# Kernel optimization log

Measured on AMD Instinct MI355X. Metric: run time of the kernel, lower is better.

## Reference

```python
import jax, jax.numpy as jnp
import numpy as np

# Static conv config (matches init_kwargs)
STRIDE = (1, 1, 1)
PAD = (1, 1, 1)
DIL = (1, 1, 1)
DG = 1  # deformable groups


def setup_inputs() -> dict:
    key = jax.random.key(0)
    k1, k2, k3 = jax.random.split(key, 3)
    N, Cin, T, H, W = 2, 32, 8, 56, 56
    Cout, kT, kH, kW = 64, 3, 3, 3
    x = jax.random.normal(k1, (N, Cin, T, H, W), dtype=jnp.float32)
    # offset channels = DG * 3 * kT*kH*kW = 81 ; layout [N, dg*K*3, To, Ho, Wo]
    offset = jax.random.normal(k2, (N, DG * 3 * kT * kH * kW, T, H, W), dtype=jnp.float32)
    stdv = 1.0 / np.sqrt(Cin * kT * kH * kW)
    weight = jax.random.uniform(k3, (Cout, Cin, kT, kH, kW), dtype=jnp.float32, minval=-stdv, maxval=stdv)
    bias = jnp.zeros((Cout,), dtype=jnp.float32)
    return {"x": x, "offset": offset, "weight": weight, "bias": bias}


def _deform_conv3d(x, offset, weight, bias):
    N, C, T, H, W = x.shape
    Co, _, kT, kH, kW = weight.shape
    K = kT * kH * kW
    st, sh, sw = STRIDE
    pt_, ph_, pw_ = PAD
    dt_, dh_, dw_ = DIL
    To = (T + 2 * pt_ - (dt_ * (kT - 1) + 1)) // st + 1
    Ho = (H + 2 * ph_ - (dh_ * (kH - 1) + 1)) // sh + 1
    Wo = (W + 2 * pw_ - (dw_ * (kW - 1) + 1)) // sw + 1
    Cg = C // DG
    # offsets: [N, DG, K, 3(dt,dh,dw), To, Ho, Wo]
    off = offset.reshape(N, DG, K, 3, To, Ho, Wo)
    kt, kh, kw = [g.reshape(-1) for g in jnp.meshgrid(
        jnp.arange(kT), jnp.arange(kH), jnp.arange(kW), indexing='ij')]
    # base sampling grid per kernel tap: [K, To, Ho, Wo] via broadcasting
    bt = (jnp.arange(To) * st - pt_)[None, :, None, None] + (kt * dt_)[:, None, None, None]
    bh = (jnp.arange(Ho) * sh - ph_)[None, None, :, None] + (kh * dh_)[:, None, None, None]
    bw = (jnp.arange(Wo) * sw - pw_)[None, None, None, :] + (kw * dw_)[:, None, None, None]
    # fractional sampling positions: [N, DG, K, To, Ho, Wo]
    pt = bt[None, None] + off[:, :, :, 0]
    ph = bh[None, None] + off[:, :, :, 1]
    pw = bw[None, None] + off[:, :, :, 2]
    t0f, h0f, w0f = jnp.floor(pt), jnp.floor(ph), jnp.floor(pw)
    lt, lh, lw = pt - t0f, ph - h0f, pw - w0f
    t0 = t0f.astype(jnp.int32)
    h0 = h0f.astype(jnp.int32)
    w0 = w0f.astype(jnp.int32)
    x_flat = x.reshape(N, DG, Cg, T * H * W)
    acc = jnp.zeros((N, DG, Cg, K, To, Ho, Wo), dtype=x.dtype)
    for ct in (0, 1):
        ti = t0 + ct
        wt = lt if ct else (1.0 - lt)
        for ch in (0, 1):
            hi = h0 + ch
            wh = lh if ch else (1.0 - lh)
            for cw in (0, 1):
                wi = w0 + cw
                ww = lw if cw else (1.0 - lw)
                valid = ((ti >= 0) & (ti < T) & (hi >= 0) & (hi < H) & (wi >= 0) & (wi < W))
                idx = (jnp.clip(ti, 0, T - 1) * H + jnp.clip(hi, 0, H - 1)) * W + jnp.clip(wi, 0, W - 1)
                v = jnp.take_along_axis(x_flat, idx.reshape(N, DG, 1, -1), axis=3)
                v = v.reshape(N, DG, Cg, K, To, Ho, Wo)
                wgt = (wt * wh * ww * valid.astype(x.dtype))[:, :, None]  # [N,DG,1,K,To,Ho,Wo]
                acc = acc + v * wgt
    w_r = weight.reshape(Co, DG, Cg, K)
    out = jnp.einsum('ogck,ngcktuv->notuv', w_r, acc)
    if bias.size > 0:
        out = out + bias[None, :, None, None, None]
    return out


def reference(x, offset, weight, bias):
    return _deform_conv3d(x, offset, weight, bias)
```

## Files before the change

### kernel.cpp

```cpp
#include <hip/hip_runtime.h>
#include <hip/hip_fp16.h>

#define CIN   32
#define COUT  64
#define TT    8
#define HH    56
#define WW    56
#define KK    27
#define SP    (TT * HH * WW)
#define NB    2
#define NBLK  784
#define DBLK  1568
#define KSPLIT 14

typedef __attribute__((ext_vector_type(8))) _Float16 half8;
typedef __attribute__((ext_vector_type(4))) float    f32x4;

#define WF_OFF   0
#define XTH_OFF  (128 << 10)

__global__ __launch_bounds__(256) void prep_kernel(const float* __restrict__ x,
                                                   const float* __restrict__ w,
                                                   __half* __restrict__ xTh,
                                                   __half* __restrict__ wf) {
    const int b = blockIdx.x;
    const int t = threadIdx.x;
    if (b < NBLK) {
        __shared__ float sm[CIN][65];
        const int s0 = b * 64, n = s0 / SP, sp0 = s0 % SP;
#pragma unroll
        for (int it = 0; it < 8; ++it) {
            const int idx = it * 256 + t, c = idx >> 6, l = idx & 63;
            sm[c][l] = x[((size_t)n * CIN + c) * SP + sp0 + l];
        }
        __syncthreads();
#pragma unroll
        for (int it = 0; it < 4; ++it) {
            const int idx = it * 256 + t, l = idx >> 4, cp = idx & 15;
            ((__half2*)xTh)[((size_t)n * SP + sp0 + l) * (CIN / 2) + cp] =
                __floats2half2_rn(sm[2 * cp][l], sm[2 * cp + 1][l]);
        }
    } else {
        const int k = b - NBLK;
#pragma unroll
        for (int it = 0; it < 8; ++it) {
            const int idx  = it * 256 + t;
            const int j    = idx & 7;
            const int lane = (idx >> 3) & 63;
            const int ct   = (idx >> 9) & 3;
            const int co   = ct * 16 + (lane & 15);
            const int c    = (lane >> 4) * 8 + j;
            wf[(((size_t)k * 4 + ct) * 64 + lane) * 8 + j] =
                __float2half(w[((size_t)co * CIN + c) * KK + k]);
        }
    }
}

__global__ __launch_bounds__(256, 4) void dconv3d_kernel(const __half* __restrict__ xTh,
                                                         const float* __restrict__ off,
                                                         const __half* __restrict__ wf,
                                                         const float* __restrict__ bias,
                                                         float* __restrict__ out) {
    __shared__ __align__(16) char smem[81 * 32 * 4];
    float (*offs)[32] = reinterpret_cast<float(*)[32]>(smem);
    float (*cmb)[2][64] = reinterpret_cast<float(*)[2][64]>(smem);

    const int t    = threadIdx.x;
    const int lane = t & 63;
    const int wv   = t >> 6;
    const int wpos = wv & 1;
    const int half = wv >> 1;

    const int posI = lane >> 2;
    const int cgI  = lane & 3;
    const int jg   = lane >> 4;

    const int bp_addr = (((lane & 15) << 2) | jg) << 2;

    const int sb  = (blockIdx.x & 7) * 196 + (blockIdx.x >> 3);
    const int s0  = sb * 32;
    const int n   = s0 / SP;
    const int spb = s0 % SP;

    {
        const float* offbase = off + ((size_t)n * (3 * KK)) * SP + spb;
        for (int i = t; i < 81 * 8; i += 256) {
            const int row = i >> 3, q = i & 7;
            *(float4*)&offs[row][q * 4] = *(const float4*)(offbase + (size_t)row * SP + q * 4);
        }
    }
    __syncthreads();

    const int sp = spb + wpos * 16 + posI;
    const int to = sp / (HH * WW);
    const int hw = sp % (HH * WW);
    const int ho = hw / WW;
    const int wo = hw % WW;
    const int pl = wpos * 16 + posI;

    f32x4 acc[4];
#pragma unroll
    for (int ct = 0; ct < 4; ++ct)
#pragma unroll
        for (int r = 0; r < 4; ++r)
            acc[ct][r] = half ? 0.f : bias[ct * 16 + jg * 4 + r];

    const __half* xn = xTh + (size_t)n * SP * CIN;

    auto tap = [&](int k) {
        const int kt  = k / 9;
        const int khh = (k / 3) % 3;
        const int kww = k % 3;

        const float pt_ = (float)(to - 1 + kt)  + offs[k * 3 + 0][pl];
        const float ph_ = (float)(ho - 1 + khh) + offs[k * 3 + 1][pl];
        const float pw_ = (float)(wo - 1 + kww) + offs[k * 3 + 2][pl];

        const float ft = floorf(pt_), fh = floorf(ph_), fw = floorf(pw_);
        const float lt = pt_ - ft, lh = ph_ - fh, lw = pw_ - fw;
        const int t0 = (int)ft, h0 = (int)fh, w0 = (int)fw;
        const int t1 = t0 + 1, h1 = h0 + 1, w1 = w0 + 1;

        float awt[2], awh[2], aww[2];
        int   it2[2], ih2[2], iw2[2];
        awt[0] = ((unsigned)t0 < TT) ? (1.f - lt) : 0.f;
        awt[1] = ((unsigned)t1 < TT) ? lt : 0.f;
        it2[0] = min(max(t0, 0), TT - 1);  it2[1] = min(max(t1, 0), TT - 1);
        awh[0] = ((unsigned)h0 < HH) ? (1.f - lh) : 0.f;
        awh[1] = ((unsigned)h1 < HH) ? lh : 0.f;
        ih2[0] = min(max(h0, 0), HH - 1);  ih2[1] = min(max(h1, 0), HH - 1);
        aww[0] = ((unsigned)w0 < WW) ? (1.f - lw) : 0.f;
        aww[1] = ((unsigned)w1 < WW) ? lw : 0.f;
        iw2[0] = min(max(w0, 0), WW - 1);  iw2[1] = min(max(w1, 0), WW - 1);

        const int dT   = (it2[1] - it2[0]) * (HH * WW);
        const int dH   = (ih2[1] - ih2[0]) * WW;
        const int dW   = iw2[1] - iw2[0];
        const int base = (it2[0] * HH + ih2[0]) * WW + iw2[0];

        int   a[8];
        float cw[8];
        a[0] = base;           a[1] = base + dW;
        a[2] = base + dH;      a[3] = a[2] + dW;
        a[4] = base + dT;      a[5] = a[4] + dW;
        a[6] = a[4] + dH;      a[7] = a[6] + dW;
#pragma unroll
        for (int ci = 0; ci < 8; ++ci) {
            const int i0 = ci >> 2, i1 = (ci >> 1) & 1, i2 = ci & 1;
            cw[ci] = awt[i0] * awh[i1] * aww[i2];
        }

        float4 g[8];
#pragma unroll
        for (int ci = 0; ci < 8; ++ci)
            g[ci] = *(const float4*)(xn + (size_t)a[ci] * CIN + cgI * 8);

        __half2 vacc[4];
#pragma unroll
        for (int j = 0; j < 4; ++j) vacc[j] = __floats2half2_rn(0.f, 0.f);
#pragma unroll
        for (int ci = 0; ci < 8; ++ci) {
            const __half2* uh = (const __half2*)&g[ci];
            const __half2 cw2 = __float2half2_rn(cw[ci]);
            vacc[0] = __hfma2(cw2, uh[0], vacc[0]);
            vacc[1] = __hfma2(cw2, uh[1], vacc[1]);
            vacc[2] = __hfma2(cw2, uh[2], vacc[2]);
            vacc[3] = __hfma2(cw2, uh[3], vacc[3]);
        }

        union { __half2 h2[4]; int i[4]; half8 h8; } u, v;
#pragma unroll
        for (int d = 0; d < 4; ++d) u.h2[d] = vacc[d];
#pragma unroll
        for (int d = 0; d < 4; ++d)
            v.i[d] = __builtin_amdgcn_ds_bpermute(bp_addr, u.i[d]);
        const half8 bfrag = v.h8;

#pragma unroll
        for (int ct = 0; ct < 4; ++ct) {
            const half8 af = *(const half8*)(wf + (((size_t)k * 4 + ct) * 64 + lane) * 8);
            acc[ct] = __builtin_amdgcn_mfma_f32_16x16x32_f16(af, bfrag, acc[ct], 0, 0, 0);
        }
    };

    if (half == 0) {
#pragma unroll
        for (int k = 0; k < KSPLIT; ++k) tap(k);
    } else {
#pragma unroll
        for (int k = KSPLIT; k < KK; ++k) tap(k);
    }

    __syncthreads();
    if (half == 1) {
#pragma unroll
        for (int ct = 0; ct < 4; ++ct)
#pragma unroll
            for (int r = 0; r < 4; ++r) cmb[ct * 4 + r][wpos][lane] = acc[ct][r];
    }
    __syncthreads();
    if (half == 0) {
#pragma unroll
        for (int ct = 0; ct < 4; ++ct)
#pragma unroll
            for (int r = 0; r < 4; ++r) {
                const int co = ct * 16 + jg * 4 + r;
                out[((size_t)n * COUT + co) * SP + spb + wpos * 16 + (lane & 15)] =
                    acc[ct][r] + cmb[ct * 4 + r][wpos][lane];
            }
    }
}

extern "C" void kernel_launch(void* const* d_in, const int* in_sizes, int n_in,
                              void* d_out, int out_size, void* d_ws, size_t ws_size,
                              hipStream_t stream) {
    const float* x    = (const float*)d_in[0];
    const float* off  = (const float*)d_in[1];
    const float* w    = (const float*)d_in[2];
    const float* bias = (const float*)d_in[3];
    float* out        = (float*)d_out;

    __half* wf  = (__half*)((char*)d_ws + WF_OFF);
    __half* xTh = (__half*)((char*)d_ws + XTH_OFF);

    prep_kernel<<<NBLK + KK, 256, 0, stream>>>(x, w, xTh, wf);
    dconv3d_kernel<<<DBLK, 256, 0, stream>>>(xTh, off, wf, bias, out);
}
```

Measured before the change: 120.4 us.

## Split taps four ways per 16-position block and drop bpermute transpose

Each block now covers 16 output positions instead of 32, and its four waves each handle about a quarter of the 27 kernel taps. The grid doubles to 3136 blocks. Lanes now gather channels directly in the MFMA B-fragment layout (position = lane&15, channel group = lane>>4), which removes the ds_bpermute shuffle. The cost is a three-way LDS reduction at the end, more offset loads per output position, and uneven tap counts across waves (7,7,7,6).

```diff
diff --git a/kernel.cpp b/kernel.cpp
--- a/kernel.cpp
+++ b/kernel.cpp
@@ -10,8 +10,7 @@
 #define SP    (TT * HH * WW)
 #define NB    2
 #define NBLK  784
-#define DBLK  1568
-#define KSPLIT 14
+#define DBLK  3136
 
 typedef __attribute__((ext_vector_type(8))) _Float16 half8;
 typedef __attribute__((ext_vector_type(4))) float    f32x4;
@@ -61,49 +60,43 @@
                                                          const __half* __restrict__ wf,
                                                          const float* __restrict__ bias,
                                                          float* __restrict__ out) {
-    __shared__ __align__(16) char smem[81 * 32 * 4];
-    float (*offs)[32] = reinterpret_cast<float(*)[32]>(smem);
-    float (*cmb)[2][64] = reinterpret_cast<float(*)[2][64]>(smem);
+    __shared__ __align__(16) char smem[3 * 16 * 64 * 4];
+    float (*offs)[16]     = reinterpret_cast<float(*)[16]>(smem);
+    float (*cmb)[16][64]  = reinterpret_cast<float(*)[16][64]>(smem);
 
     const int t    = threadIdx.x;
     const int lane = t & 63;
-    const int wv   = t >> 6;
-    const int wpos = wv & 1;
-    const int half = wv >> 1;
-
-    const int posI = lane >> 2;
-    const int cgI  = lane & 3;
+    const int q    = t >> 6;
+
+    const int posI = lane & 15;
     const int jg   = lane >> 4;
 
-    const int bp_addr = (((lane & 15) << 2) | jg) << 2;
-
-    const int sb  = (blockIdx.x & 7) * 196 + (blockIdx.x >> 3);
-    const int s0  = sb * 32;
+    const int sb  = (blockIdx.x & 7) * 392 + (blockIdx.x >> 3);
+    const int s0  = sb * 16;
     const int n   = s0 / SP;
     const int spb = s0 % SP;
 
     {
         const float* offbase = off + ((size_t)n * (3 * KK)) * SP + spb;
-        for (int i = t; i < 81 * 8; i += 256) {
-            const int row = i >> 3, q = i & 7;
-            *(float4*)&offs[row][q * 4] = *(const float4*)(offbase + (size_t)row * SP + q * 4);
+        for (int i = t; i < 81 * 4; i += 256) {
+            const int row = i >> 2, qd = i & 3;
+            *(float4*)&offs[row][qd * 4] = *(const float4*)(offbase + (size_t)row * SP + qd * 4);
         }
     }
     __syncthreads();
 
-    const int sp = spb + wpos * 16 + posI;
+    const int sp = spb + posI;
     const int to = sp / (HH * WW);
     const int hw = sp % (HH * WW);
     const int ho = hw / WW;
     const int wo = hw % WW;
-    const int pl = wpos * 16 + posI;
 
     f32x4 acc[4];
 #pragma unroll
     for (int ct = 0; ct < 4; ++ct)
 #pragma unroll
         for (int r = 0; r < 4; ++r)
-            acc[ct][r] = half ? 0.f : bias[ct * 16 + jg * 4 + r];
+            acc[ct][r] = (q == 0) ? bias[ct * 16 + jg * 4 + r] : 0.f;
 
     const __half* xn = xTh + (size_t)n * SP * CIN;
 
@@ -112,9 +105,9 @@
         const int khh = (k / 3) % 3;
         const int kww = k % 3;
 
-        const float pt_ = (float)(to - 1 + kt)  + offs[k * 3 + 0][pl];
-        const float ph_ = (float)(ho - 1 + khh) + offs[k * 3 + 1][pl];
-        const float pw_ = (float)(wo - 1 + kww) + offs[k * 3 + 2][pl];
+        const float pt_ = (float)(to - 1 + kt)  + offs[k * 3 + 0][posI];
+        const float ph_ = (float)(ho - 1 + khh) + offs[k * 3 + 1][posI];
+        const float pw_ = (float)(wo - 1 + kww) + offs[k * 3 + 2][posI];
 
         const float ft = floorf(pt_), fh = floorf(ph_), fw = floorf(pw_);
         const float lt = pt_ - ft, lh = ph_ - fh, lw = pw_ - fw;
@@ -153,28 +146,21 @@
         float4 g[8];
 #pragma unroll
         for (int ci = 0; ci < 8; ++ci)
-            g[ci] = *(const float4*)(xn + (size_t)a[ci] * CIN + cgI * 8);
-
-        __half2 vacc[4];
-#pragma unroll
-        for (int j = 0; j < 4; ++j) vacc[j] = __floats2half2_rn(0.f, 0.f);
+            g[ci] = *(const float4*)(xn + (size_t)a[ci] * CIN + jg * 8);
+
+        union { __half2 h2[4]; half8 h8; } u;
+        u.h2[0] = __floats2half2_rn(0.f, 0.f);
+        u.h2[1] = u.h2[0]; u.h2[2] = u.h2[0]; u.h2[3] = u.h2[0];
 #pragma unroll
         for (int ci = 0; ci < 8; ++ci) {
             const __half2* uh = (const __half2*)&g[ci];
             const __half2 cw2 = __float2half2_rn(cw[ci]);
-            vacc[0] = __hfma2(cw2, uh[0], vacc[0]);
-            vacc[1] = __hfma2(cw2, uh[1], vacc[1]);
-            vacc[2] = __hfma2(cw2, uh[2], vacc[2]);
-            vacc[3] = __hfma2(cw2, uh[3], vacc[3]);
-        }
-
-        union { __half2 h2[4]; int i[4]; half8 h8; } u, v;
-#pragma unroll
-        for (int d = 0; d < 4; ++d) u.h2[d] = vacc[d];
-#pragma unroll
-        for (int d = 0; d < 4; ++d)
-            v.i[d] = __builtin_amdgcn_ds_bpermute(bp_addr, u.i[d]);
-        const half8 bfrag = v.h8;
+            u.h2[0] = __hfma2(cw2, uh[0], u.h2[0]);
+            u.h2[1] = __hfma2(cw2, uh[1], u.h2[1]);
+            u.h2[2] = __hfma2(cw2, uh[2], u.h2[2]);
+            u.h2[3] = __hfma2(cw2, uh[3], u.h2[3]);
+        }
+        const half8 bfrag = u.h8;
 
 #pragma unroll
         for (int ct = 0; ct < 4; ++ct) {
@@ -183,30 +169,37 @@
         }
     };
 
-    if (half == 0) {
-#pragma unroll
-        for (int k = 0; k < KSPLIT; ++k) tap(k);
+    if (q == 0) {
+#pragma unroll
+        for (int k = 0; k < 7; ++k) tap(k);
+    } else if (q == 1) {
+#pragma unroll
+        for (int k = 7; k < 14; ++k) tap(k);
+    } else if (q == 2) {
+#pragma unroll
+        for (int k = 14; k < 21; ++k) tap(k);
     } else {
 #pragma unroll
-        for (int k = KSPLIT; k < KK; ++k) tap(k);
+        for (int k = 21; k < KK; ++k) tap(k);
     }
 
     __syncthreads();
-    if (half == 1) {
+    if (q != 0) {
 #pragma unroll
         for (int ct = 0; ct < 4; ++ct)
 #pragma unroll
-            for (int r = 0; r < 4; ++r) cmb[ct * 4 + r][wpos][lane] = acc[ct][r];
+            for (int r = 0; r < 4; ++r) cmb[q - 1][ct * 4 + r][lane] = acc[ct][r];
     }
     __syncthreads();
-    if (half == 0) {
+    if (q == 0) {
 #pragma unroll
         for (int ct = 0; ct < 4; ++ct)
 #pragma unroll
             for (int r = 0; r < 4; ++r) {
                 const int co = ct * 16 + jg * 4 + r;
-                out[((size_t)n * COUT + co) * SP + spb + wpos * 16 + (lane & 15)] =
-                    acc[ct][r] + cmb[ct * 4 + r][wpos][lane];
+                const int i  = ct * 4 + r;
+                out[((size_t)n * COUT + co) * SP + spb + posI] =
+                    acc[ct][r] + cmb[0][i][lane] + cmb[1][i][lane] + cmb[2][i][lane];
             }
     }
 }
```

Measured after the change: 144.0 us. 1.2x slower.
